# Kernel tuning notes

Hardware: AMD Instinct MI355X
Metric: run time of the kernel (lower is better)

Reference implementation:

```python
import jax, jax.numpy as jnp
import numpy as np

TEMPERATURE = 8.0  # sqrt(d_k), d_k = 64
B, L, D = 32, 2048, 64


def setup_inputs() -> dict:
    key = jax.random.key(0)
    kq, kk, kv, kd, km = jax.random.split(key, 5)
    q = jax.random.normal(kq, (B, L, D), dtype=jnp.float32)
    k = jax.random.normal(kk, (B, L, D), dtype=jnp.float32)
    v = jax.random.normal(kv, (B, L, D), dtype=jnp.float32)
    diag_mask = jax.random.randint(kd, (B, L, L), 0, 2, dtype=jnp.int32)
    mask = jax.random.randint(km, (B, L, L), 0, 2).astype(jnp.bool_)
    return {"q": q, "k": k, "v": v, "diag_mask": diag_mask, "mask": mask}


def reference(q, k, v, diag_mask, mask):
    # attn = (q @ k^T) / temperature              [B, L, L]
    attn = jnp.einsum("bqd,bkd->bqk", q, k) / TEMPERATURE
    # optional mask: masked_fill(mask, -inf)
    attn = jnp.where(mask, -jnp.inf, attn)
    # diag mask: masked_fill(diag_mask == 0, -1e32)
    attn = jnp.where(diag_mask == 0, jnp.float32(-1e32), attn)
    attn = jax.nn.softmax(attn, axis=-1)
    # output = attn @ v                            [B, L, D]
    output = jnp.einsum("bqk,bkd->bqd", attn, v)
    return (output, attn)
```

## Files before the change

kernel.cpp:

```cpp
#include <hip/hip_runtime.h>
#include <cstdint>
#include <cstddef>

#define BB 32
#define LL 2048
#define DD 64
#define NKB 16

#define BIG_NEG (-3.0e38f)

__global__ __launch_bounds__(256) void k_scores(
    const float* __restrict__ q, const float* __restrict__ kmat,
    const int* __restrict__ diag, const int* __restrict__ mask,
    float* __restrict__ attn, float* __restrict__ pm, float* __restrict__ pl)
{
    __shared__ __align__(16) float sQT[32][156];
    __shared__ __align__(16) float sKT[32][156];

    const int b  = blockIdx.z;
    const int q0 = blockIdx.y * 128;
    const int k0 = blockIdx.x * 128;
    const int t  = threadIdx.x;
    const int tx = t & 15;
    const int ty = t >> 4;
    const int tyb = ty * 8;
    const int txb = tx * 4;

    const float* qb = q    + ((size_t)b * LL + q0) * DD;
    const float* kb = kmat + ((size_t)b * LL + k0) * DD;

    float acc[8][8];
    #pragma unroll
    for (int i = 0; i < 8; ++i)
        #pragma unroll
        for (int j = 0; j < 8; ++j) acc[i][j] = 0.0f;

    for (int dc = 0; dc < DD; dc += 32) {
        #pragma unroll
        for (int i = 0; i < 4; ++i) {
            int lin = t + 256 * i;
            int row = lin >> 3;
            int dv  = lin & 7;
            int cc  = row + dv * 4;
            float4 a = *(const float4*)(qb + (size_t)row * DD + dc + dv * 4);
            sQT[dv * 4 + 0][cc] = a.x;
            sQT[dv * 4 + 1][cc] = a.y;
            sQT[dv * 4 + 2][cc] = a.z;
            sQT[dv * 4 + 3][cc] = a.w;
            float4 c4 = *(const float4*)(kb + (size_t)row * DD + dc + dv * 4);
            sKT[dv * 4 + 0][cc] = c4.x;
            sKT[dv * 4 + 1][cc] = c4.y;
            sKT[dv * 4 + 2][cc] = c4.z;
            sKT[dv * 4 + 3][cc] = c4.w;
        }
        __syncthreads();

        #pragma unroll
        for (int d = 0; d < 32; ++d) {
            const int rot = d & 28;
            float4 a0 = *(const float4*)&sQT[d][tyb + rot];
            float4 a1 = *(const float4*)&sQT[d][tyb + 4 + rot];
            float4 b0 = *(const float4*)&sKT[d][txb + rot];
            float4 b1 = *(const float4*)&sKT[d][txb + 64 + rot];
            float aa[8] = {a0.x, a0.y, a0.z, a0.w, a1.x, a1.y, a1.z, a1.w};
            float bb[8] = {b0.x, b0.y, b0.z, b0.w, b1.x, b1.y, b1.z, b1.w};
            #pragma unroll
            for (int ri = 0; ri < 8; ++ri)
                #pragma unroll
                for (int ci = 0; ci < 8; ++ci)
                    acc[ri][ci] = fmaf(aa[ri], bb[ci], acc[ri][ci]);
        }
        __syncthreads();
    }

    #pragma unroll
    for (int ri = 0; ri < 8; ++ri) {
        int qq = q0 + tyb + ri;
        size_t rb    = ((size_t)b * LL + qq) * LL + k0;
        size_t base0 = rb + txb;
        size_t base1 = rb + txb + 64;
        int4 dm0 = *(const int4*)(diag + base0);
        int4 dm1 = *(const int4*)(diag + base1);
        int4 mk0 = *(const int4*)(mask + base0);
        int4 mk1 = *(const int4*)(mask + base1);
        int dmv[8] = {dm0.x, dm0.y, dm0.z, dm0.w, dm1.x, dm1.y, dm1.z, dm1.w};
        int mkv[8] = {mk0.x, mk0.y, mk0.z, mk0.w, mk1.x, mk1.y, mk1.z, mk1.w};
        float o[8];
        #pragma unroll
        for (int ci = 0; ci < 8; ++ci) {
            float s = acc[ri][ci] * 0.125f;
            o[ci] = (dmv[ci] == 0 || mkv[ci] != 0) ? BIG_NEG : s;
        }
        *(float4*)(attn + base0) = make_float4(o[0], o[1], o[2], o[3]);
        *(float4*)(attn + base1) = make_float4(o[4], o[5], o[6], o[7]);

        if (pm != nullptr) {
            float rm = fmaxf(fmaxf(fmaxf(o[0], o[1]), fmaxf(o[2], o[3])),
                             fmaxf(fmaxf(o[4], o[5]), fmaxf(o[6], o[7])));
            #pragma unroll
            for (int off = 8; off >= 1; off >>= 1)
                rm = fmaxf(rm, __shfl_xor(rm, off, 64));
            float rs = 0.0f;
            #pragma unroll
            for (int ci = 0; ci < 8; ++ci) rs += __expf(o[ci] - rm);
            #pragma unroll
            for (int off = 8; off >= 1; off >>= 1)
                rs += __shfl_xor(rs, off, 64);
            if (tx == 0) {
                size_t pidx = ((size_t)b * LL + qq) * NKB + blockIdx.x;
                pm[pidx] = rm;
                pl[pidx] = rs;
            }
        }
    }
}

__global__ __launch_bounds__(256) void k_reduce(
    const float* __restrict__ pm, const float* __restrict__ pl,
    float2* __restrict__ stats)
{
    int row = blockIdx.x * 256 + threadIdx.x;
    const float4* m4 = (const float4*)(pm + (size_t)row * NKB);
    const float4* l4 = (const float4*)(pl + (size_t)row * NKB);
    float4 m0 = m4[0], m1 = m4[1], m2 = m4[2], m3 = m4[3];
    float4 l0 = l4[0], l1 = l4[1], l2 = l4[2], l3 = l4[3];
    float m = fmaxf(fmaxf(fmaxf(fmaxf(m0.x, m0.y), fmaxf(m0.z, m0.w)),
                          fmaxf(fmaxf(m1.x, m1.y), fmaxf(m1.z, m1.w))),
                    fmaxf(fmaxf(fmaxf(m2.x, m2.y), fmaxf(m2.z, m2.w)),
                          fmaxf(fmaxf(m3.x, m3.y), fmaxf(m3.z, m3.w))));
    float l = l0.x * __expf(m0.x - m) + l0.y * __expf(m0.y - m)
            + l0.z * __expf(m0.z - m) + l0.w * __expf(m0.w - m)
            + l1.x * __expf(m1.x - m) + l1.y * __expf(m1.y - m)
            + l1.z * __expf(m1.z - m) + l1.w * __expf(m1.w - m)
            + l2.x * __expf(m2.x - m) + l2.y * __expf(m2.y - m)
            + l2.z * __expf(m2.z - m) + l2.w * __expf(m2.w - m)
            + l3.x * __expf(m3.x - m) + l3.y * __expf(m3.y - m)
            + l3.z * __expf(m3.z - m) + l3.w * __expf(m3.w - m);
    stats[row] = make_float2(m, 1.0f / l);
}

__global__ __launch_bounds__(256) void k_rowstats(
    const float* __restrict__ attn, float2* __restrict__ stats)
{
    __shared__ float redm[4];
    __shared__ float reds[4];
    const float* p = attn + (size_t)blockIdx.x * LL;
    const int t = threadIdx.x;
    const int wave = t >> 6, lane = t & 63;

    float4 x0 = ((const float4*)p)[t];
    float4 x1 = ((const float4*)p)[t + 256];

    float m = fmaxf(fmaxf(fmaxf(x0.x, x0.y), fmaxf(x0.z, x0.w)),
                    fmaxf(fmaxf(x1.x, x1.y), fmaxf(x1.z, x1.w)));
    #pragma unroll
    for (int off = 32; off >= 1; off >>= 1)
        m = fmaxf(m, __shfl_xor(m, off, 64));
    if (lane == 0) redm[wave] = m;
    __syncthreads();
    m = fmaxf(fmaxf(redm[0], redm[1]), fmaxf(redm[2], redm[3]));

    float s = __expf(x0.x - m) + __expf(x0.y - m)
            + __expf(x0.z - m) + __expf(x0.w - m)
            + __expf(x1.x - m) + __expf(x1.y - m)
            + __expf(x1.z - m) + __expf(x1.w - m);
    #pragma unroll
    for (int off = 32; off >= 1; off >>= 1)
        s += __shfl_xor(s, off, 64);
    if (lane == 0) reds[wave] = s;
    __syncthreads();
    s = (reds[0] + reds[1]) + (reds[2] + reds[3]);

    if (t == 0) stats[blockIdx.x] = make_float2(m, 1.0f / s);
}

__global__ __launch_bounds__(256) void k_softmax(float* __restrict__ attn)
{
    __shared__ float redm[4];
    __shared__ float reds[4];
    float* p = attn + (size_t)blockIdx.x * LL;
    const int t = threadIdx.x;
    const int wave = t >> 6, lane = t & 63;

    float4 x0 = ((const float4*)p)[t];
    float4 x1 = ((const float4*)p)[t + 256];

    float m = fmaxf(fmaxf(fmaxf(x0.x, x0.y), fmaxf(x0.z, x0.w)),
                    fmaxf(fmaxf(x1.x, x1.y), fmaxf(x1.z, x1.w)));
    #pragma unroll
    for (int off = 32; off >= 1; off >>= 1)
        m = fmaxf(m, __shfl_xor(m, off, 64));
    if (lane == 0) redm[wave] = m;
    __syncthreads();
    m = fmaxf(fmaxf(redm[0], redm[1]), fmaxf(redm[2], redm[3]));

    x0.x = expf(x0.x - m); x0.y = expf(x0.y - m);
    x0.z = expf(x0.z - m); x0.w = expf(x0.w - m);
    x1.x = expf(x1.x - m); x1.y = expf(x1.y - m);
    x1.z = expf(x1.z - m); x1.w = expf(x1.w - m);

    float s = (x0.x + x0.y + x0.z + x0.w) + (x1.x + x1.y + x1.z + x1.w);
    #pragma unroll
    for (int off = 32; off >= 1; off >>= 1)
        s += __shfl_xor(s, off, 64);
    if (lane == 0) reds[wave] = s;
    __syncthreads();
    s = (reds[0] + reds[1]) + (reds[2] + reds[3]);

    float inv = 1.0f / s;
    x0.x *= inv; x0.y *= inv; x0.z *= inv; x0.w *= inv;
    x1.x *= inv; x1.y *= inv; x1.z *= inv; x1.w *= inv;
    ((float4*)p)[t]       = x0;
    ((float4*)p)[t + 256] = x1;
}

__global__ __launch_bounds__(256) void k_pv_softmax(
    float* __restrict__ attn, const float* __restrict__ v,
    const float2* __restrict__ stats, float* __restrict__ out)
{
    __shared__ __align__(16) float sPT[64][188];
    __shared__ __align__(16) float sV[64][68];
    __shared__ float sM[128];
    __shared__ float sIL[128];

    const int b  = blockIdx.y;
    const int q0 = blockIdx.x * 128;
    const int t  = threadIdx.x;
    const int tx = t & 15;
    const int ty = t >> 4;
    const int tyb = ty * 8;
    const int txb = tx * 4;

    float* pb = attn + ((size_t)b * LL + q0) * LL;
    const float* vb = v + (size_t)b * LL * DD;

    if (stats != nullptr && t < 128) {
        float2 st = stats[(size_t)b * LL + q0 + t];
        sM[t]  = st.x;
        sIL[t] = st.y;
    }
    __syncthreads();

    float acc[8][4];
    #pragma unroll
    for (int i = 0; i < 8; ++i)
        #pragma unroll
        for (int j = 0; j < 4; ++j) acc[i][j] = 0.0f;

    for (int k0 = 0; k0 < LL; k0 += 64) {
        #pragma unroll
        for (int i = 0; i < 8; ++i) {
            int lin = t + 256 * i;
            int row = lin >> 4;
            int kv  = lin & 15;
            float* src = pb + (size_t)row * LL + k0 + kv * 4;
            float4 a = *(const float4*)src;
            if (stats != nullptr) {
                float m  = sM[row];
                float il = sIL[row];
                a.x = __expf(a.x - m) * il;
                a.y = __expf(a.y - m) * il;
                a.z = __expf(a.z - m) * il;
                a.w = __expf(a.w - m) * il;
                *(float4*)src = a;
            }
            int cc = row + kv * 4;
            sPT[kv * 4 + 0][cc] = a.x;
            sPT[kv * 4 + 1][cc] = a.y;
            sPT[kv * 4 + 2][cc] = a.z;
            sPT[kv * 4 + 3][cc] = a.w;
        }
        #pragma unroll
        for (int i = 0; i < 4; ++i) {
            int lin = t + 256 * i;
            int row = lin >> 4;
            int dv  = lin & 15;
            *(float4*)&sV[row][dv * 4] =
                *(const float4*)(vb + (size_t)(k0 + row) * DD + dv * 4);
        }
        __syncthreads();

        #pragma unroll
        for (int kk = 0; kk < 64; ++kk) {
            const int rot = kk & 60;
            float4 a0 = *(const float4*)&sPT[kk][tyb + rot];
            float4 a1 = *(const float4*)&sPT[kk][tyb + 4 + rot];
            float4 b0 = *(const float4*)&sV[kk][txb];
            float aa[8] = {a0.x, a0.y, a0.z, a0.w, a1.x, a1.y, a1.z, a1.w};
            float bb[4] = {b0.x, b0.y, b0.z, b0.w};
            #pragma unroll
            for (int ri = 0; ri < 8; ++ri)
                #pragma unroll
                for (int ci = 0; ci < 4; ++ci)
                    acc[ri][ci] = fmaf(aa[ri], bb[ci], acc[ri][ci]);
        }
        __syncthreads();
    }

    #pragma unroll
    for (int ri = 0; ri < 8; ++ri) {
        float4 o = make_float4(acc[ri][0], acc[ri][1], acc[ri][2], acc[ri][3]);
        *(float4*)(out + ((size_t)b * LL + q0 + tyb + ri) * DD + txb) = o;
    }
}

extern "C" void kernel_launch(void* const* d_in, const int* in_sizes, int n_in,
                              void* d_out, int out_size, void* d_ws, size_t ws_size,
                              hipStream_t stream)
{
    const float* q    = (const float*)d_in[0];
    const float* k    = (const float*)d_in[1];
    const float* v    = (const float*)d_in[2];
    const int*   diag = (const int*)d_in[3];
    const int*   mask = (const int*)d_in[4];

    float* out  = (float*)d_out;
    float* attn = out + (size_t)BB * LL * DD;

    const size_t ROWS = (size_t)BB * LL;
    const size_t PART_FLOATS = ROWS * NKB;
    const size_t needA = PART_FLOATS * 4 * 2 + ROWS * 8;
    const size_t needB = ROWS * 8;

    if (d_ws != nullptr && ws_size >= needA) {
        float*  pm    = (float*)d_ws;
        float*  pl    = pm + PART_FLOATS;
        float2* stats = (float2*)(pl + PART_FLOATS);
        k_scores    <<<dim3(LL / 128, LL / 128, BB), 256, 0, stream>>>(
                        q, k, diag, mask, attn, pm, pl);
        k_reduce    <<<dim3((int)(ROWS / 256)),       256, 0, stream>>>(pm, pl, stats);
        k_pv_softmax<<<dim3(LL / 128, BB),            256, 0, stream>>>(attn, v, stats, out);
    } else if (d_ws != nullptr && ws_size >= needB) {
        float2* stats = (float2*)d_ws;
        k_scores    <<<dim3(LL / 128, LL / 128, BB), 256, 0, stream>>>(
                        q, k, diag, mask, attn, nullptr, nullptr);
        k_rowstats  <<<dim3(BB * LL),                 256, 0, stream>>>(attn, stats);
        k_pv_softmax<<<dim3(LL / 128, BB),            256, 0, stream>>>(attn, v, stats, out);
    } else {
        k_scores    <<<dim3(LL / 128, LL / 128, BB), 256, 0, stream>>>(
                        q, k, diag, mask, attn, nullptr, nullptr);
        k_softmax   <<<dim3(BB * LL),                 256, 0, stream>>>(attn);
        k_pv_softmax<<<dim3(LL / 128, BB),            256, 0, stream>>>(attn, v, nullptr, out);
    }
}
```

Baseline: 1.878 ms.

## Prefetch mask tiles during QK^T and pipeline PV with smaller row tiles

In the scores kernel, the diag and mask int4 loads for the first rows are issued before the second d-chunk of the dot product, and later rows are prefetched two iterations ahead inside the epilogue. The kernel also gets a launch-bounds occupancy hint. The PV/softmax kernel drops from 128 to 64 query rows per block, which doubles the grid, and register-prefetches the next P and V tiles while the current tile is computed. It is also templated on whether stats are present. The aim is to hide global-memory latency on the mask reads and the attention re-read/write, at the cost of more live registers and less reuse of V per block.

```diff
diff --git a/kernel.cpp b/kernel.cpp
--- a/kernel.cpp
+++ b/kernel.cpp
@@ -9,7 +9,7 @@
 
 #define BIG_NEG (-3.0e38f)
 
-__global__ __launch_bounds__(256) void k_scores(
+__global__ __launch_bounds__(256, 3) void k_scores(
     const float* __restrict__ q, const float* __restrict__ kmat,
     const int* __restrict__ diag, const int* __restrict__ mask,
     float* __restrict__ attn, float* __restrict__ pm, float* __restrict__ pl)
@@ -35,6 +35,9 @@
         #pragma unroll
         for (int j = 0; j < 8; ++j) acc[i][j] = 0.0f;
 
+    int4 dm0v[8], dm1v[8], mk0v[8], mk1v[8];
+
+    #pragma unroll
     for (int dc = 0; dc < DD; dc += 32) {
         #pragma unroll
         for (int i = 0; i < 4; ++i) {
@@ -55,6 +58,18 @@
         }
         __syncthreads();
 
+        if (dc == 32) {
+            #pragma unroll
+            for (int r = 0; r < 2; ++r) {
+                int qq = q0 + tyb + r;
+                size_t base = ((size_t)b * LL + qq) * LL + k0 + txb;
+                dm0v[r] = *(const int4*)(diag + base);
+                dm1v[r] = *(const int4*)(diag + base + 64);
+                mk0v[r] = *(const int4*)(mask + base);
+                mk1v[r] = *(const int4*)(mask + base + 64);
+            }
+        }
+
         #pragma unroll
         for (int d = 0; d < 32; ++d) {
             const int rot = d & 28;
@@ -79,12 +94,20 @@
         size_t rb    = ((size_t)b * LL + qq) * LL + k0;
         size_t base0 = rb + txb;
         size_t base1 = rb + txb + 64;
-        int4 dm0 = *(const int4*)(diag + base0);
-        int4 dm1 = *(const int4*)(diag + base1);
-        int4 mk0 = *(const int4*)(mask + base0);
-        int4 mk1 = *(const int4*)(mask + base1);
-        int dmv[8] = {dm0.x, dm0.y, dm0.z, dm0.w, dm1.x, dm1.y, dm1.z, dm1.w};
-        int mkv[8] = {mk0.x, mk0.y, mk0.z, mk0.w, mk1.x, mk1.y, mk1.z, mk1.w};
+
+        if (ri < 6) {
+            int qq2 = q0 + tyb + ri + 2;
+            size_t b2 = ((size_t)b * LL + qq2) * LL + k0 + txb;
+            dm0v[ri + 2] = *(const int4*)(diag + b2);
+            dm1v[ri + 2] = *(const int4*)(diag + b2 + 64);
+            mk0v[ri + 2] = *(const int4*)(mask + b2);
+            mk1v[ri + 2] = *(const int4*)(mask + b2 + 64);
+        }
+
+        int dmv[8] = {dm0v[ri].x, dm0v[ri].y, dm0v[ri].z, dm0v[ri].w,
+                      dm1v[ri].x, dm1v[ri].y, dm1v[ri].z, dm1v[ri].w};
+        int mkv[8] = {mk0v[ri].x, mk0v[ri].y, mk0v[ri].z, mk0v[ri].w,
+                      mk1v[ri].x, mk1v[ri].y, mk1v[ri].z, mk1v[ri].w};
         float o[8];
         #pragma unroll
         for (int ci = 0; ci < 8; ++ci) {
@@ -214,93 +237,120 @@
     ((float4*)p)[t + 256] = x1;
 }
 
-__global__ __launch_bounds__(256) void k_pv_softmax(
+template <bool HAVE_STATS>
+__global__ __launch_bounds__(256, 3) void k_pv_softmax(
     float* __restrict__ attn, const float* __restrict__ v,
     const float2* __restrict__ stats, float* __restrict__ out)
 {
-    __shared__ __align__(16) float sPT[64][188];
+    __shared__ __align__(16) float sPT[64][124];
     __shared__ __align__(16) float sV[64][68];
-    __shared__ float sM[128];
-    __shared__ float sIL[128];
+    __shared__ float sM[64];
+    __shared__ float sIL[64];
 
     const int b  = blockIdx.y;
-    const int q0 = blockIdx.x * 128;
+    const int q0 = blockIdx.x * 64;
     const int t  = threadIdx.x;
     const int tx = t & 15;
     const int ty = t >> 4;
-    const int tyb = ty * 8;
-    const int txb = tx * 4;
 
     float* pb = attn + ((size_t)b * LL + q0) * LL;
     const float* vb = v + (size_t)b * LL * DD;
 
-    if (stats != nullptr && t < 128) {
-        float2 st = stats[(size_t)b * LL + q0 + t];
-        sM[t]  = st.x;
-        sIL[t] = st.y;
-    }
-    __syncthreads();
-
-    float acc[8][4];
-    #pragma unroll
-    for (int i = 0; i < 8; ++i)
+    if (HAVE_STATS) {
+        if (t < 64) {
+            float2 st = stats[(size_t)b * LL + q0 + t];
+            sM[t]  = st.x;
+            sIL[t] = st.y;
+        }
+        __syncthreads();
+    }
+
+    float mrow[4], ilrow[4];
+    if (HAVE_STATS) {
+        #pragma unroll
+        for (int i = 0; i < 4; ++i) {
+            mrow[i]  = sM[ty + 16 * i];
+            ilrow[i] = sIL[ty + 16 * i];
+        }
+    }
+
+    float acc[4][4];
+    #pragma unroll
+    for (int i = 0; i < 4; ++i)
         #pragma unroll
         for (int j = 0; j < 4; ++j) acc[i][j] = 0.0f;
 
-    for (int k0 = 0; k0 < LL; k0 += 64) {
-        #pragma unroll
-        for (int i = 0; i < 8; ++i) {
-            int lin = t + 256 * i;
-            int row = lin >> 4;
-            int kv  = lin & 15;
-            float* src = pb + (size_t)row * LL + k0 + kv * 4;
-            float4 a = *(const float4*)src;
-            if (stats != nullptr) {
-                float m  = sM[row];
-                float il = sIL[row];
+    float4 rp[4], rv[4];
+    #pragma unroll
+    for (int i = 0; i < 4; ++i) {
+        rp[i] = *(const float4*)(pb + (size_t)(ty + 16 * i) * LL + 4 * tx);
+        rv[i] = *(const float4*)(vb + (size_t)(ty + 16 * i) * DD + 4 * tx);
+    }
+
+    for (int c = 0; c < 32; ++c) {
+        const int k0 = c * 64;
+
+        float4 pw[4];
+        #pragma unroll
+        for (int i = 0; i < 4; ++i) {
+            int row = ty + 16 * i;
+            float4 a = rp[i];
+            if (HAVE_STATS) {
+                float m  = mrow[i];
+                float il = ilrow[i];
                 a.x = __expf(a.x - m) * il;
                 a.y = __expf(a.y - m) * il;
                 a.z = __expf(a.z - m) * il;
                 a.w = __expf(a.w - m) * il;
-                *(float4*)src = a;
-            }
-            int cc = row + kv * 4;
-            sPT[kv * 4 + 0][cc] = a.x;
-            sPT[kv * 4 + 1][cc] = a.y;
-            sPT[kv * 4 + 2][cc] = a.z;
-            sPT[kv * 4 + 3][cc] = a.w;
-        }
-        #pragma unroll
-        for (int i = 0; i < 4; ++i) {
-            int lin = t + 256 * i;
-            int row = lin >> 4;
-            int dv  = lin & 15;
-            *(float4*)&sV[row][dv * 4] =
-                *(const float4*)(vb + (size_t)(k0 + row) * DD + dv * 4);
-        }
-        __syncthreads();
-
-        #pragma unroll
-        for (int kk = 0; kk < 64; ++kk) {
-            const int rot = kk & 60;
-            float4 a0 = *(const float4*)&sPT[kk][tyb + rot];
-            float4 a1 = *(const float4*)&sPT[kk][tyb + 4 + rot];
-            float4 b0 = *(const float4*)&sV[kk][txb];
-            float aa[8] = {a0.x, a0.y, a0.z, a0.w, a1.x, a1.y, a1.z, a1.w};
-            float bb[4] = {b0.x, b0.y, b0.z, b0.w};
-            #pragma unroll
-            for (int ri = 0; ri < 8; ++ri)
+            }
+            pw[i] = a;
+            int cc = row + 4 * tx;
+            sPT[4 * tx + 0][cc] = a.x;
+            sPT[4 * tx + 1][cc] = a.y;
+            sPT[4 * tx + 2][cc] = a.z;
+            sPT[4 * tx + 3][cc] = a.w;
+            *(float4*)&sV[row][4 * tx] = rv[i];
+        }
+        __syncthreads();
+
+        if (c < 31) {
+            const int k1 = k0 + 64;
+            #pragma unroll
+            for (int i = 0; i < 4; ++i) {
+                rp[i] = *(const float4*)(pb + (size_t)(ty + 16 * i) * LL + k1 + 4 * tx);
+                rv[i] = *(const float4*)(vb + (size_t)(k1 + ty + 16 * i) * DD + 4 * tx);
+            }
+        }
+        if (HAVE_STATS) {
+            #pragma unroll
+            for (int i = 0; i < 4; ++i)
+                *(float4*)(pb + (size_t)(ty + 16 * i) * LL + k0 + 4 * tx) = pw[i];
+        }
+
+        #pragma unroll
+        for (int kg = 0; kg < 16; ++kg) {
+            const int rot = 4 * kg;
+            #pragma unroll
+            for (int c2 = 0; c2 < 4; ++c2) {
+                const int kk = 4 * kg + c2;
+                float4 a0 = *(const float4*)&sPT[kk][4 * ty + rot];
+                float4 b0 = *(const float4*)&sV[kk][4 * tx];
+                float aa[4] = {a0.x, a0.y, a0.z, a0.w};
+                float bb[4] = {b0.x, b0.y, b0.z, b0.w};
                 #pragma unroll
-                for (int ci = 0; ci < 4; ++ci)
-                    acc[ri][ci] = fmaf(aa[ri], bb[ci], acc[ri][ci]);
-        }
-        __syncthreads();
-    }
-
-    #pragma unroll
-    for (int ri = 0; ri < 8; ++ri) {
+                for (int ri = 0; ri < 4; ++ri)
+                    #pragma unroll
+                    for (int ci = 0; ci < 4; ++ci)
+                        acc[ri][ci] = fmaf(aa[ri], bb[ci], acc[ri][ci]);
+            }
+        }
+        __syncthreads();
+    }
+
+    #pragma unroll
+    for (int ri = 0; ri < 4; ++ri) {
         float4 o = make_float4(acc[ri][0], acc[ri][1], acc[ri][2], acc[ri][3]);
-        *(float4*)(out + ((size_t)b * LL + q0 + tyb + ri) * DD + txb) = o;
+        *(float4*)(out + ((size_t)b * LL + q0 + 4 * ty + ri) * DD + 4 * tx) = o;
     }
 }
 
@@ -326,20 +376,20 @@
         float*  pm    = (float*)d_ws;
         float*  pl    = pm + PART_FLOATS;
         float2* stats = (float2*)(pl + PART_FLOATS);
-        k_scores    <<<dim3(LL / 128, LL / 128, BB), 256, 0, stream>>>(
-                        q, k, diag, mask, attn, pm, pl);
-        k_reduce    <<<dim3((int)(ROWS / 256)),       256, 0, stream>>>(pm, pl, stats);
-        k_pv_softmax<<<dim3(LL / 128, BB),            256, 0, stream>>>(attn, v, stats, out);
+        k_scores<<<dim3(LL / 128, LL / 128, BB), 256, 0, stream>>>(
+            q, k, diag, mask, attn, pm, pl);
+        k_reduce<<<dim3((int)(ROWS / 256)), 256, 0, stream>>>(pm, pl, stats);
+        k_pv_softmax<true><<<dim3(LL / 64, BB), 256, 0, stream>>>(attn, v, stats, out);
     } else if (d_ws != nullptr && ws_size >= needB) {
         float2* stats = (float2*)d_ws;
-        k_scores    <<<dim3(LL / 128, LL / 128, BB), 256, 0, stream>>>(
-                        q, k, diag, mask, attn, nullptr, nullptr);
-        k_rowstats  <<<dim3(BB * LL),                 256, 0, stream>>>(attn, stats);
-        k_pv_softmax<<<dim3(LL / 128, BB),            256, 0, stream>>>(attn, v, stats, out);
+        k_scores<<<dim3(LL / 128, LL / 128, BB), 256, 0, stream>>>(
+            q, k, diag, mask, attn, nullptr, nullptr);
+        k_rowstats<<<dim3(BB * LL), 256, 0, stream>>>(attn, stats);
+        k_pv_softmax<true><<<dim3(LL / 64, BB), 256, 0, stream>>>(attn, v, stats, out);
     } else {
-        k_scores    <<<dim3(LL / 128, LL / 128, BB), 256, 0, stream>>>(
-                        q, k, diag, mask, attn, nullptr, nullptr);
-        k_softmax   <<<dim3(BB * LL),                 256, 0, stream>>>(attn);
-        k_pv_softmax<<<dim3(LL / 128, BB),            256, 0, stream>>>(attn, v, nullptr, out);
-    }
-}
+        k_scores<<<dim3(LL / 128, LL / 128, BB), 256, 0, stream>>>(
+            q, k, diag, mask, attn, nullptr, nullptr);
+        k_softmax<<<dim3(BB * LL), 256, 0, stream>>>(attn);
+        k_pv_softmax<false><<<dim3(LL / 64, BB), 256, 0, stream>>>(attn, v, nullptr, out);
+    }
+}
```

After: 2.013 ms. 1.07x slower.
